# Kernel tuning notes

Hardware: AMD Instinct MI355X
Metric: run time of the kernel (lower is better)

The kernel has to match this reference:

```python
import jax, jax.numpy as jnp
import numpy as np

EPS = 1e-5  # torch BatchNorm default eps
B, C, T, NOUT, NCLS = 4096, 32, 512, 16, 4


def setup_inputs() -> dict:
    key = jax.random.key(0)
    ks = jax.random.split(key, 12)
    s = lambda k, shape: jax.random.normal(k, shape, jnp.float32) * 0.05
    return {
        "de": jax.random.normal(ks[0], (B, C, T), jnp.float32),
        "adj": jax.random.normal(ks[1], (B, C, C), jnp.float32),  # unused by forward (module recomputes corr)
        "dw_w": s(ks[2], (C, 1, 3)),      # depthwise Conv1d weight [C,1,3]
        "dw_b": s(ks[3], (C,)),
        "pw_w": s(ks[4], (C, C)),          # pointwise 1x1 conv [out,in]
        "pw_b": s(ks[5], (C,)),
        "bn1_g": jnp.ones((C,), jnp.float32),
        "bn1_b": jnp.zeros((C,), jnp.float32),
        "gc_w": s(ks[6], (T, NOUT)),       # GraphConvolution weight
        "fc_w": s(ks[7], (C * NOUT, C)),   # fc62 Linear(512,32)
        "fc_b": s(ks[8], (C,)),
        "bn2_g": jnp.ones((C,), jnp.float32),
        "bn2_b": jnp.zeros((C,), jnp.float32),
        "cls_w": s(ks[9], (C, NCLS)),      # fcclass Linear(32,4)
        "cls_b": s(ks[10], (NCLS,)),
    }


def reference(de, adj, dw_w, dw_b, pw_w, pw_b, bn1_g, bn1_b, gc_w,
              fc_w, fc_b, bn2_g, bn2_b, cls_w, cls_b):
    # --- SeparableConv2d (really 1d): depthwise k=3 -> pointwise 1x1 -> BN -> relu ---
    x = jax.lax.conv_general_dilated(
        de, dw_w, window_strides=(1,), padding=[(1, 1)],
        dimension_numbers=("NCH", "OIH", "NCH"),
        feature_group_count=de.shape[1]) + dw_b[None, :, None]
    x = jnp.einsum("oc,bct->bot", pw_w, x) + pw_b[None, :, None]
    m = x.mean((0, 2), keepdims=True)
    v = x.var((0, 2), keepdims=True)  # biased, as BN normalization uses
    x = (x - m) / jnp.sqrt(v + EPS) * bn1_g[None, :, None] + bn1_b[None, :, None]
    x = jax.nn.relu(x)                       # [B, C, T]

    # --- batched Pearson corrcoef over the time axis (vectorizes the per-sample loop) ---
    xt = x.transpose(0, 2, 1)                # [B, T, C]
    Tn = xt.shape[1]
    f = (Tn - 1) / Tn
    xc = xt - xt.mean(1, keepdims=True)
    num = jnp.einsum("btn,btm->bnm", xc, xc) / Tn   # biased covariance
    var = xt.var(1, ddof=1)                         # torch var default unbiased
    den = jnp.sqrt(var[:, :, None] * var[:, None, :]) * f
    cor = num / den                          # [B, C, C]

    # --- Chebyshev graph convolution (single K term, adj = cor) + relu ---
    g = jnp.einsum("bnm,bmt->bnt", cor, x)   # message passing over channel graph
    g = jax.nn.relu(jnp.einsum("bnt,to->bno", g, gc_w))  # [B, C, 16]

    # --- fc62: Linear -> BN1d -> (dropout: identity) -> sigmoid ---
    h = g.reshape(g.shape[0], -1) @ fc_w + fc_b          # [B, 32]
    m2 = h.mean(0)
    v2 = h.var(0)
    h = (h - m2) / jnp.sqrt(v2 + EPS) * bn2_g + bn2_b
    h = jax.nn.sigmoid(h)

    return h @ cls_w + cls_b                 # [B, 4]
```

## Files before the change

kernel.cpp:

```cpp
#include <hip/hip_runtime.h>
#include <math.h>

#define BB 4096
#define CC 32
#define TT 512
#define NOUTC 16
#define EPSF 1e-5f
#define XS 520


typedef __attribute__((ext_vector_type(16))) float f32x16;
typedef __attribute__((ext_vector_type(4)))  float f32x4;
typedef __attribute__((ext_vector_type(8)))  short short8;
typedef __attribute__((ext_vector_type(4)))  unsigned int u32x4;
typedef __attribute__((ext_vector_type(4)))  float vf4;
typedef vf4 __attribute__((aligned(4))) vf4u;

__device__ __forceinline__ unsigned short f2b(float f) {
  unsigned int u = __builtin_bit_cast(unsigned int, f);
  return (unsigned short)((u + 0x7FFFu + ((u >> 16) & 1u)) >> 16);
}
__device__ __forceinline__ float blo(unsigned int u) {
  return __builtin_bit_cast(float, u << 16);
}
__device__ __forceinline__ float bhi(unsigned int u) {
  return __builtin_bit_cast(float, u & 0xFFFF0000u);
}
__device__ __forceinline__ unsigned int pk2(float a, float b) {
  return (unsigned int)f2b(a) | ((unsigned int)f2b(b) << 16);
}

__device__ __forceinline__ void conv_cols(const float* __restrict__ deb,
    const float* __restrict__ dw, const float* __restrict__ db_,
    int tid, float* x1A, float* x1B) {
  int t0 = tid * 2;
  int off = (tid == 0) ? 0 : ((tid == 255) ? t0 - 2 : t0 - 1);
#pragma unroll
  for (int c = 0; c < CC; c++) {
    vf4u v = *reinterpret_cast<const vf4u*>(deb + c * TT + off);
    float vm1 = (tid == 0) ? 0.f : ((tid == 255) ? v.y : v.x);
    float v0  = (tid == 0) ? v.x : ((tid == 255) ? v.z : v.y);
    float vp1 = (tid == 0) ? v.y : ((tid == 255) ? v.w : v.z);
    float vp2 = (tid == 0) ? v.z : ((tid == 255) ? 0.f : v.w);
    float w0 = dw[c * 3], w1 = dw[c * 3 + 1], w2 = dw[c * 3 + 2], bc = db_[c];
    x1A[c] = fmaf(w0, vm1, fmaf(w1, v0, fmaf(w2, vp1, bc)));
    x1B[c] = fmaf(w0, v0, fmaf(w1, vp1, fmaf(w2, vp2, bc)));
  }
}

__device__ __forceinline__ void stage_row(unsigned short* lds1, int XHo, int XLo,
                                          int row, const float* x) {
#pragma unroll
  for (int cb = 0; cb < 4; cb++) {
    u32x4 hv, lv;
#pragma unroll
    for (int k = 0; k < 4; k++) {
      float a = x[cb * 8 + 2 * k], b2 = x[cb * 8 + 2 * k + 1];
      unsigned int ua = __builtin_bit_cast(unsigned int, a);
      unsigned int ub = __builtin_bit_cast(unsigned int, b2);
      hv[k] = (ua >> 16) | (ub & 0xFFFF0000u);
      float ra = a - __builtin_bit_cast(float, ua & 0xFFFF0000u);
      float rb = b2 - __builtin_bit_cast(float, ub & 0xFFFF0000u);
      lv[k] = pk2(ra, rb);
    }
    *(u32x4*)&lds1[XHo + row * 40 + cb * 8] = hv;
    *(u32x4*)&lds1[XLo + row * 40 + cb * 8] = lv;
  }
}

__global__ __launch_bounds__(256) void k1_stats(const float* __restrict__ de,
    const float* __restrict__ dw, const float* __restrict__ db_,
    const float* __restrict__ pw, const float* __restrict__ pwb,
    float* __restrict__ part, unsigned int* __restrict__ x2h, int useWs) {
  __shared__ __align__(16) unsigned short lds1[39168];
  const int XHo = 0, XLo = 10240, X2Bo = 20480, PWHo = 37120, PWLo = 38144;

  int tid = threadIdx.x, b = blockIdx.x;
  int lane = tid & 63, w = tid >> 6;
  int m31 = lane & 31, kh = lane >> 5;

  const float* deb = de + (size_t)b * CC * TT;
  float x1A[CC], x1B[CC];
  conv_cols(deb, dw, db_, tid, x1A, x1B);

  for (int i = tid; i < CC * CC; i += 256) {
    float v = pw[i];
    unsigned int u = __builtin_bit_cast(unsigned int, v);
    lds1[PWHo + i] = (unsigned short)(u >> 16);
    float r = v - __builtin_bit_cast(float, u & 0xFFFF0000u);
    lds1[PWLo + i] = f2b(r);
  }
  __syncthreads();

  short8 ah[2], al[2];
#pragma unroll
  for (int s = 0; s < 2; s++) {
    ah[s] = *(const short8*)&lds1[PWHo + m31 * 32 + s * 16 + kh * 8];
    al[s] = *(const short8*)&lds1[PWLo + m31 * 32 + s * 16 + kh * 8];
  }
  float pbv[16];
#pragma unroll
  for (int r = 0; r < 16; r++) pbv[r] = pwb[(r & 3) + 8 * (r >> 2) + 4 * kh];

#pragma unroll
  for (int h = 0; h < 2; h++) {
    if ((tid >> 7) == h) {
      int lr = 2 * (tid & 127);
      stage_row(lds1, XHo, XLo, lr, x1A);
      stage_row(lds1, XHo, XLo, lr + 1, x1B);
    }
    __syncthreads();

#pragma unroll
    for (int i = 0; i < 2; i++) {
      int wt = w * 2 + i;
      f32x16 acc;
#pragma unroll
      for (int r = 0; r < 16; r++) acc[r] = 0.f;
      int rowb = wt * 32 + m31;
#pragma unroll
      for (int s = 0; s < 2; s++) {
        short8 bh = *(const short8*)&lds1[XHo + rowb * 40 + s * 16 + kh * 8];
        short8 bl = *(const short8*)&lds1[XLo + rowb * 40 + s * 16 + kh * 8];
        acc = __builtin_amdgcn_mfma_f32_32x32x16_bf16(ah[s], bh, acc, 0, 0, 0);
        acc = __builtin_amdgcn_mfma_f32_32x32x16_bf16(ah[s], bl, acc, 0, 0, 0);
        acc = __builtin_amdgcn_mfma_f32_32x32x16_bf16(al[s], bh, acc, 0, 0, 0);
      }
      int t = h * 256 + wt * 32 + m31;
#pragma unroll
      for (int pr = 0; pr < 8; pr++) {
        int o0 = ((2 * pr) & 3) + 8 * (pr >> 1) + 4 * kh;
        unsigned int p = pk2(acc[2 * pr] + pbv[2 * pr], acc[2 * pr + 1] + pbv[2 * pr + 1]);
        lds1[X2Bo + o0 * 520 + t] = (unsigned short)(p & 0xFFFFu);
        lds1[X2Bo + (o0 + 1) * 520 + t] = (unsigned short)(p >> 16);
      }
    }
    __syncthreads();
  }

  unsigned int* xw = x2h + (size_t)b * (CC * 256);
  int L = tid & 63;
#pragma unroll
  for (int it = 0; it < 8; it++) {
    int o = it * 4 + w;
    u32x4 v = *(const u32x4*)&lds1[X2Bo + o * 520 + L * 8];
    float s = 0.f, q = 0.f;
#pragma unroll
    for (int k = 0; k < 4; k++) {
      float a = blo(v[k]), c2 = bhi(v[k]);
      s += a + c2;
      q = fmaf(a, a, fmaf(c2, c2, q));
    }
#pragma unroll
    for (int d = 1; d < 64; d <<= 1) { s += __shfl_xor(s, d); q += __shfl_xor(q, d); }
    if (L == 0) {
      part[(size_t)o * BB + b] = s;
      part[(size_t)(32 + o) * BB + b] = q;
    }
    if (useWs) *(u32x4*)(xw + (size_t)(it * 256 + tid) * 4) = v;
  }
}

__global__ void k2_bn1(const float* __restrict__ part, const float* __restrict__ g,
                       const float* __restrict__ bta, float* __restrict__ ws) {
  __shared__ float redS[256], redQ[256];
  int o = blockIdx.x, tid = threadIdx.x;
  const float* ps = part + (size_t)o * BB;
  const float* pq = part + (size_t)(CC + o) * BB;
  float s = 0, q = 0;
  for (int i = tid; i < BB; i += 256) { s += ps[i]; q += pq[i]; }
  redS[tid] = s; redQ[tid] = q;
  __syncthreads();
  for (int k = 128; k > 0; k >>= 1) {
    if (tid < k) { redS[tid] += redS[tid + k]; redQ[tid] += redQ[tid + k]; }
    __syncthreads();
  }
  if (tid == 0) {
    float N = (float)BB * (float)TT;
    float mean = redS[0] / N;
    float var = redQ[0] / N - mean * mean;
    float sc = g[o] / sqrtf(var + EPSF);
    ws[o] = sc;
    ws[32 + o] = bta[o] - mean * sc;
  }
}

__global__ __launch_bounds__(256) void k3_main(const float* __restrict__ de,
    const float* __restrict__ dw, const float* __restrict__ db_,
    const float* __restrict__ pw, const float* __restrict__ pwb,
    const float* __restrict__ ws, const float* __restrict__ gcw,
    const float* __restrict__ fcw, const float* __restrict__ fcb,
    float* __restrict__ hT, const unsigned int* __restrict__ x2h, int useWs) {
  __shared__ __align__(16) unsigned short x_s[CC * XS];
  __shared__ __align__(16) unsigned short gc_s[NOUTC * XS];
  __shared__ float gramP[2][CC * CC];
  __shared__ float zP[2][CC * NOUTC];
  __shared__ float num_s[CC * 33];
  __shared__ float red16[CC * 8];
  __shared__ float mu_s[CC], inv_s[CC];
  __shared__ float Zi_s[CC * NOUTC];
  __shared__ float g2_s[CC * NOUTC];
  __shared__ float red2[CC * 9];

  int tid = threadIdx.x, b = blockIdx.x;
  int w = tid >> 6, lane = tid & 63;
  int t0 = tid * 2;

  for (int i = tid; i < TT * NOUTC; i += 256) {
    int t = i >> 4, o = i & 15;
    gc_s[o * XS + t] = f2b(gcw[i]);
  }

  if (useWs) {
    const unsigned int* xr = x2h + (size_t)b * CC * 256;
#pragma unroll
    for (int o = 0; o < CC; o++) {
      unsigned int u = xr[o * 256 + tid];
      float sc = ws[o], sh = ws[32 + o];
      unsigned short hA = f2b(fmaxf(fmaf(blo(u), sc, sh), 0.f));
      unsigned short hB = f2b(fmaxf(fmaf(bhi(u), sc, sh), 0.f));
      *(unsigned int*)(&x_s[o * XS + t0]) = (unsigned int)hA | ((unsigned int)hB << 16);
    }
  } else {
    const float* deb = de + (size_t)b * CC * TT;
    float x1A[CC], x1B[CC];
    conv_cols(deb, dw, db_, tid, x1A, x1B);
#pragma unroll
    for (int o = 0; o < CC; o++) {
      float aA = pwb[o], aB = pwb[o];
#pragma unroll
      for (int c = 0; c < CC; c++) { float pv = pw[o * CC + c]; aA = fmaf(pv, x1A[c], aA); aB = fmaf(pv, x1B[c], aB); }
      float sc = ws[o], sh = ws[32 + o];
      unsigned short hA = f2b(fmaxf(fmaf(aA, sc, sh), 0.f));
      unsigned short hB = f2b(fmaxf(fmaf(aB, sc, sh), 0.f));
      *(unsigned int*)(&x_s[o * XS + t0]) = (unsigned int)hA | ((unsigned int)hB << 16);
    }
  }
  __syncthreads();

  {
    int c = tid >> 3, j = tid & 7;
    float s = 0.f;
#pragma unroll
    for (int it = 0; it < 8; it++) {
      u32x4 u = *reinterpret_cast<const u32x4*>(&x_s[c * XS + j * 64 + it * 8]);
#pragma unroll
      for (int k = 0; k < 4; k++) s += blo(u[k]) + bhi(u[k]);
    }
    red16[c * 8 + j] = s;
  }

  if (w < 2) {
    int m = lane & 31, kh = lane >> 5;
    f32x16 acc;
#pragma unroll
    for (int r = 0; r < 16; r++) acc[r] = 0.f;
    int kbase = w * 256 + kh * 8;
#pragma unroll
    for (int kk = 0; kk < 256; kk += 16) {
      short8 a = *(const short8*)(&x_s[m * XS + kbase + kk]);
      acc = __builtin_amdgcn_mfma_f32_32x32x16_bf16(a, a, acc, 0, 0, 0);
    }
#pragma unroll
    for (int r = 0; r < 16; r++) {
      int row = (r & 3) + 8 * (r >> 2) + 4 * kh;
      gramP[w][row * CC + m] = acc[r];
    }
  } else {
    int w2 = w - 2;
    int n16 = lane & 15, q = lane >> 4;
    f32x4 ac0, ac1;
#pragma unroll
    for (int r = 0; r < 4; r++) { ac0[r] = 0.f; ac1[r] = 0.f; }
    int kbase = w2 * 256 + q * 8;
#pragma unroll
    for (int kk = 0; kk < 256; kk += 32) {
      short8 bfr = *(const short8*)(&gc_s[n16 * XS + kbase + kk]);
      short8 af0 = *(const short8*)(&x_s[n16 * XS + kbase + kk]);
      short8 af1 = *(const short8*)(&x_s[(16 + n16) * XS + kbase + kk]);
      ac0 = __builtin_amdgcn_mfma_f32_16x16x32_bf16(af0, bfr, ac0, 0, 0, 0);
      ac1 = __builtin_amdgcn_mfma_f32_16x16x32_bf16(af1, bfr, ac1, 0, 0, 0);
    }
#pragma unroll
    for (int r = 0; r < 4; r++) {
      int row = q * 4 + r;
      zP[w2][row * NOUTC + n16] = ac0[r];
      zP[w2][(16 + row) * NOUTC + n16] = ac1[r];
    }
  }
  __syncthreads();
  if (tid < CC) {
    float s = 0.f;
#pragma unroll
    for (int j = 0; j < 8; j++) s += red16[tid * 8 + j];
    mu_s[tid] = s;
  }
  __syncthreads();
  for (int i = tid; i < CC * CC; i += 256) {
    int n = i >> 5, m = i & 31;
    num_s[n * 33 + m] = gramP[0][i] + gramP[1][i] - mu_s[n] * mu_s[m] * (1.f / (float)TT);
  }
  for (int i = tid; i < CC * NOUTC; i += 256) Zi_s[i] = zP[0][i] + zP[1][i];
  __syncthreads();
  if (tid < CC) inv_s[tid] = rsqrtf(num_s[tid * 33 + tid]);
  __syncthreads();
  for (int i = tid; i < CC * NOUTC; i += 256) {
    int n = i >> 4, o = i & 15;
    float s = 0.f;
#pragma unroll
    for (int m = 0; m < CC; m++) s = fmaf(num_s[n * 33 + m] * inv_s[m], Zi_s[m * NOUTC + o], s);
    g2_s[i] = fmaxf(s * inv_s[n], 0.f);
  }
  __syncthreads();
  {
    int j = tid & 31, ch = tid >> 5;
    float p = 0.f;
#pragma unroll
    for (int ii = 0; ii < 64; ii++) {
      int i = ch * 64 + ii;
      p = fmaf(g2_s[i], fcw[i * CC + j], p);
    }
    red2[j * 9 + ch] = p;
  }
  __syncthreads();
  if (tid < CC) {
    float h = fcb[tid];
#pragma unroll
    for (int ch = 0; ch < 8; ch++) h += red2[tid * 9 + ch];
    hT[(size_t)tid * BB + b] = h;
  }
}

__global__ void k4_bn2(const float* __restrict__ hT, const float* __restrict__ g,
                       const float* __restrict__ bta, float* __restrict__ ws) {
  __shared__ float redS[256], redQ[256];
  int j = blockIdx.x, tid = threadIdx.x;
  const float* row = hT + (size_t)j * BB;
  float s = 0, q = 0;
  for (int i = tid; i < BB; i += 256) { float v = row[i]; s += v; q = fmaf(v, v, q); }
  redS[tid] = s; redQ[tid] = q;
  __syncthreads();
  for (int k = 128; k > 0; k >>= 1) {
    if (tid < k) { redS[tid] += redS[tid + k]; redQ[tid] += redQ[tid + k]; }
    __syncthreads();
  }
  if (tid == 0) {
    float N = (float)BB;
    float mean = redS[0] / N;
    float var = redQ[0] / N - mean * mean;
    float sc = g[j] / sqrtf(var + EPSF);
    ws[64 + j] = sc;
    ws[96 + j] = bta[j] - mean * sc;
  }
}

__global__ void k5_out(const float* __restrict__ hT, const float* __restrict__ ws,
                       const float* __restrict__ clsw, const float* __restrict__ clsb,
                       float* __restrict__ out) {
  __shared__ float hs[CC * 257];
  int b0 = blockIdx.x * 256, tid = threadIdx.x;
  for (int i = tid; i < CC * 256; i += 256) {
    int j = i >> 8, bb = i & 255;
    float v = fmaf(hT[(size_t)j * BB + b0 + bb], ws[64 + j], ws[96 + j]);
    hs[j * 257 + bb] = 1.f / (1.f + expf(-v));
  }
  __syncthreads();
  float o0 = clsb[0], o1 = clsb[1], o2 = clsb[2], o3 = clsb[3];
#pragma unroll
  for (int j = 0; j < CC; j++) {
    float h = hs[j * 257 + tid];
    o0 = fmaf(h, clsw[j * 4 + 0], o0);
    o1 = fmaf(h, clsw[j * 4 + 1], o1);
    o2 = fmaf(h, clsw[j * 4 + 2], o2);
    o3 = fmaf(h, clsw[j * 4 + 3], o3);
  }
  float4* out4 = reinterpret_cast<float4*>(out);
  out4[b0 + tid] = make_float4(o0, o1, o2, o3);
}

extern "C" void kernel_launch(void* const* d_in, const int* in_sizes, int n_in,
                              void* d_out, int out_size, void* d_ws, size_t ws_size,
                              hipStream_t stream) {
  const float* de   = (const float*)d_in[0];
  const float* dw   = (const float*)d_in[2];
  const float* db_  = (const float*)d_in[3];
  const float* pw   = (const float*)d_in[4];
  const float* pwb  = (const float*)d_in[5];
  const float* bn1g = (const float*)d_in[6];
  const float* bn1b = (const float*)d_in[7];
  const float* gcw  = (const float*)d_in[8];
  const float* fcw  = (const float*)d_in[9];
  const float* fcb  = (const float*)d_in[10];
  const float* bn2g = (const float*)d_in[11];
  const float* bn2b = (const float*)d_in[12];
  const float* clsw = (const float*)d_in[13];
  const float* clsb = (const float*)d_in[14];

  float* ws   = (float*)d_ws;
  float* hT   = ws + 128;
  float* part = ws + 131200;
  unsigned int* x2h = (unsigned int*)(ws + 393344);
  float* out  = (float*)d_out;

  size_t need = 393344ull * 4ull + (size_t)BB * CC * 256 * 4;
  int useWs = (ws_size >= need) ? 1 : 0;

  k1_stats<<<BB, 256, 0, stream>>>(de, dw, db_, pw, pwb, part, x2h, useWs);
  k2_bn1<<<CC, 256, 0, stream>>>(part, bn1g, bn1b, ws);
  k3_main<<<BB, 256, 0, stream>>>(de, dw, db_, pw, pwb, ws, gcw, fcw, fcb, hT, x2h, useWs);
  k4_bn2<<<CC, 256, 0, stream>>>(hT, bn2g, bn2b, ws);
  k5_out<<<BB / 256, 256, 0, stream>>>(hT, ws, clsw, clsb, out);
}
```

Measured before the change: 521.4 us.

## Use single fp16 MFMA for pointwise conv, shrink LDS, pre-swizzle GCN weights

The pointwise conv in k1 switches from a three-pass bf16 hi/lo split to a single fp16 MFMA pass. This cuts the MFMA count and roughly halves LDS use. The stats reduction now runs per half and writes the workspace in a half-major layout. The GCN weight is converted to bf16 once in k2, in MFMA fragment order, so k3 reads it straight into registers instead of rebuilding gc_s every block. Both big kernels trim LDS and set launch_bounds(256,3) to raise occupancy. The cost is reduced precision for the pointwise result: fp16 range and mantissa replace the near-fp32 split.

Result: faster. 487.0 us (-6.6%).

```diff
diff --git a/kernel.cpp b/kernel.cpp
--- a/kernel.cpp
+++ b/kernel.cpp
@@ -12,6 +12,7 @@
 typedef __attribute__((ext_vector_type(16))) float f32x16;
 typedef __attribute__((ext_vector_type(4)))  float f32x4;
 typedef __attribute__((ext_vector_type(8)))  short short8;
+typedef __attribute__((ext_vector_type(8)))  _Float16 half8;
 typedef __attribute__((ext_vector_type(4)))  unsigned int u32x4;
 typedef __attribute__((ext_vector_type(4)))  float vf4;
 typedef vf4 __attribute__((aligned(4))) vf4u;
@@ -28,6 +29,13 @@
 }
 __device__ __forceinline__ unsigned int pk2(float a, float b) {
   return (unsigned int)f2b(a) | ((unsigned int)f2b(b) << 16);
+}
+__device__ __forceinline__ unsigned short h16(float f) {
+  _Float16 h = (_Float16)f;
+  return __builtin_bit_cast(unsigned short, h);
+}
+__device__ __forceinline__ unsigned int h2pk(float a, float b) {
+  return (unsigned int)h16(a) | ((unsigned int)h16(b) << 16);
 }
 
 __device__ __forceinline__ void conv_cols(const float* __restrict__ deb,
@@ -48,66 +56,52 @@
   }
 }
 
-__device__ __forceinline__ void stage_row(unsigned short* lds1, int XHo, int XLo,
-                                          int row, const float* x) {
+__device__ __forceinline__ void stage_row_f16(unsigned short* lds1, int row, const float* x) {
 #pragma unroll
   for (int cb = 0; cb < 4; cb++) {
-    u32x4 hv, lv;
-#pragma unroll
-    for (int k = 0; k < 4; k++) {
-      float a = x[cb * 8 + 2 * k], b2 = x[cb * 8 + 2 * k + 1];
-      unsigned int ua = __builtin_bit_cast(unsigned int, a);
-      unsigned int ub = __builtin_bit_cast(unsigned int, b2);
-      hv[k] = (ua >> 16) | (ub & 0xFFFF0000u);
-      float ra = a - __builtin_bit_cast(float, ua & 0xFFFF0000u);
-      float rb = b2 - __builtin_bit_cast(float, ub & 0xFFFF0000u);
-      lv[k] = pk2(ra, rb);
-    }
-    *(u32x4*)&lds1[XHo + row * 40 + cb * 8] = hv;
-    *(u32x4*)&lds1[XLo + row * 40 + cb * 8] = lv;
-  }
-}
-
-__global__ __launch_bounds__(256) void k1_stats(const float* __restrict__ de,
+    u32x4 v;
+#pragma unroll
+    for (int k = 0; k < 4; k++) v[k] = h2pk(x[cb * 8 + 2 * k], x[cb * 8 + 2 * k + 1]);
+    *(u32x4*)&lds1[row * 40 + cb * 8] = v;
+  }
+}
+
+__global__ __launch_bounds__(256, 3) void k1_stats(const float* __restrict__ de,
     const float* __restrict__ dw, const float* __restrict__ db_,
     const float* __restrict__ pw, const float* __restrict__ pwb,
     float* __restrict__ part, unsigned int* __restrict__ x2h, int useWs) {
-  __shared__ __align__(16) unsigned short lds1[39168];
-  const int XHo = 0, XLo = 10240, X2Bo = 20480, PWHo = 37120, PWLo = 38144;
+  __shared__ __align__(16) unsigned short lds1[19712];
+  const int XFo = 0, X2Bo = 10240, PWFo = 18688;
 
   int tid = threadIdx.x, b = blockIdx.x;
   int lane = tid & 63, w = tid >> 6;
   int m31 = lane & 31, kh = lane >> 5;
+  int hw = tid >> 5, l32 = tid & 31;
 
   const float* deb = de + (size_t)b * CC * TT;
   float x1A[CC], x1B[CC];
   conv_cols(deb, dw, db_, tid, x1A, x1B);
 
-  for (int i = tid; i < CC * CC; i += 256) {
-    float v = pw[i];
-    unsigned int u = __builtin_bit_cast(unsigned int, v);
-    lds1[PWHo + i] = (unsigned short)(u >> 16);
-    float r = v - __builtin_bit_cast(float, u & 0xFFFF0000u);
-    lds1[PWLo + i] = f2b(r);
-  }
-  __syncthreads();
-
-  short8 ah[2], al[2];
-#pragma unroll
-  for (int s = 0; s < 2; s++) {
-    ah[s] = *(const short8*)&lds1[PWHo + m31 * 32 + s * 16 + kh * 8];
-    al[s] = *(const short8*)&lds1[PWLo + m31 * 32 + s * 16 + kh * 8];
-  }
+  for (int i = tid; i < CC * CC; i += 256) lds1[PWFo + i] = h16(pw[i]);
+  __syncthreads();
+
+  half8 ah[2];
+#pragma unroll
+  for (int s = 0; s < 2; s++)
+    ah[s] = *(const half8*)&lds1[PWFo + m31 * 32 + s * 16 + kh * 8];
   float pbv[16];
 #pragma unroll
   for (int r = 0; r < 16; r++) pbv[r] = pwb[(r & 3) + 8 * (r >> 2) + 4 * kh];
+
+  unsigned int* xw = x2h + (size_t)b * (CC * 256);
+  float sAcc[4] = {0.f, 0.f, 0.f, 0.f}, qAcc[4] = {0.f, 0.f, 0.f, 0.f};
 
 #pragma unroll
   for (int h = 0; h < 2; h++) {
     if ((tid >> 7) == h) {
       int lr = 2 * (tid & 127);
-      stage_row(lds1, XHo, XLo, lr, x1A);
-      stage_row(lds1, XHo, XLo, lr + 1, x1B);
+      stage_row_f16(lds1, lr, x1A);
+      stage_row_f16(lds1, lr + 1, x1B);
     }
     __syncthreads();
 
@@ -120,51 +114,60 @@
       int rowb = wt * 32 + m31;
 #pragma unroll
       for (int s = 0; s < 2; s++) {
-        short8 bh = *(const short8*)&lds1[XHo + rowb * 40 + s * 16 + kh * 8];
-        short8 bl = *(const short8*)&lds1[XLo + rowb * 40 + s * 16 + kh * 8];
-        acc = __builtin_amdgcn_mfma_f32_32x32x16_bf16(ah[s], bh, acc, 0, 0, 0);
-        acc = __builtin_amdgcn_mfma_f32_32x32x16_bf16(ah[s], bl, acc, 0, 0, 0);
-        acc = __builtin_amdgcn_mfma_f32_32x32x16_bf16(al[s], bh, acc, 0, 0, 0);
+        half8 bh = *(const half8*)&lds1[XFo + rowb * 40 + s * 16 + kh * 8];
+        acc = __builtin_amdgcn_mfma_f32_32x32x16_f16(ah[s], bh, acc, 0, 0, 0);
       }
-      int t = h * 256 + wt * 32 + m31;
+      int tloc = wt * 32 + m31;
 #pragma unroll
       for (int pr = 0; pr < 8; pr++) {
         int o0 = ((2 * pr) & 3) + 8 * (pr >> 1) + 4 * kh;
         unsigned int p = pk2(acc[2 * pr] + pbv[2 * pr], acc[2 * pr + 1] + pbv[2 * pr + 1]);
-        lds1[X2Bo + o0 * 520 + t] = (unsigned short)(p & 0xFFFFu);
-        lds1[X2Bo + (o0 + 1) * 520 + t] = (unsigned short)(p >> 16);
+        lds1[X2Bo + o0 * 264 + tloc] = (unsigned short)(p & 0xFFFFu);
+        lds1[X2Bo + (o0 + 1) * 264 + tloc] = (unsigned short)(p >> 16);
       }
     }
     __syncthreads();
-  }
-
-  unsigned int* xw = x2h + (size_t)b * (CC * 256);
-  int L = tid & 63;
-#pragma unroll
-  for (int it = 0; it < 8; it++) {
-    int o = it * 4 + w;
-    u32x4 v = *(const u32x4*)&lds1[X2Bo + o * 520 + L * 8];
-    float s = 0.f, q = 0.f;
-#pragma unroll
-    for (int k = 0; k < 4; k++) {
-      float a = blo(v[k]), c2 = bhi(v[k]);
-      s += a + c2;
-      q = fmaf(a, a, fmaf(c2, c2, q));
-    }
-#pragma unroll
-    for (int d = 1; d < 64; d <<= 1) { s += __shfl_xor(s, d); q += __shfl_xor(q, d); }
-    if (L == 0) {
-      part[(size_t)o * BB + b] = s;
-      part[(size_t)(32 + o) * BB + b] = q;
-    }
-    if (useWs) *(u32x4*)(xw + (size_t)(it * 256 + tid) * 4) = v;
+
+#pragma unroll
+    for (int it = 0; it < 4; it++) {
+      int o = it * 8 + hw;
+      u32x4 v = *(const u32x4*)&lds1[X2Bo + o * 264 + l32 * 8];
+      float s = 0.f, q = 0.f;
+#pragma unroll
+      for (int k = 0; k < 4; k++) {
+        float a = blo(v[k]), c2 = bhi(v[k]);
+        s += a + c2;
+        q = fmaf(a, a, fmaf(c2, c2, q));
+      }
+#pragma unroll
+      for (int d = 1; d < 32; d <<= 1) { s += __shfl_xor(s, d); q += __shfl_xor(q, d); }
+      sAcc[it] += s; qAcc[it] += q;
+      if (useWs) *(u32x4*)(xw + (size_t)h * 4096 + o * 128 + l32 * 4) = v;
+    }
+  }
+
+  if (l32 == 0) {
+#pragma unroll
+    for (int it = 0; it < 4; it++) {
+      int o = it * 8 + hw;
+      part[(size_t)o * BB + b] = sAcc[it];
+      part[(size_t)(32 + o) * BB + b] = qAcc[it];
+    }
   }
 }
 
 __global__ void k2_bn1(const float* __restrict__ part, const float* __restrict__ g,
-                       const float* __restrict__ bta, float* __restrict__ ws) {
+                       const float* __restrict__ bta, float* __restrict__ ws,
+                       const float* __restrict__ gcw, unsigned short* __restrict__ gcf) {
   __shared__ float redS[256], redQ[256];
   int o = blockIdx.x, tid = threadIdx.x;
+  {
+    int i = o * 256 + tid;
+    int e = i & 7, ln = (i >> 3) & 63, j = (i >> 9) & 7, w2 = i >> 12;
+    int q = ln >> 4, n16 = ln & 15;
+    int t = w2 * 256 + q * 8 + j * 32 + e;
+    gcf[i] = f2b(gcw[t * 16 + n16]);
+  }
   const float* ps = part + (size_t)o * BB;
   const float* pq = part + (size_t)(CC + o) * BB;
   float s = 0, q = 0;
@@ -185,37 +188,28 @@
   }
 }
 
-__global__ __launch_bounds__(256) void k3_main(const float* __restrict__ de,
+__global__ __launch_bounds__(256, 3) void k3_main(const float* __restrict__ de,
     const float* __restrict__ dw, const float* __restrict__ db_,
     const float* __restrict__ pw, const float* __restrict__ pwb,
-    const float* __restrict__ ws, const float* __restrict__ gcw,
+    const float* __restrict__ ws, const unsigned short* __restrict__ gcf,
     const float* __restrict__ fcw, const float* __restrict__ fcb,
     float* __restrict__ hT, const unsigned int* __restrict__ x2h, int useWs) {
   __shared__ __align__(16) unsigned short x_s[CC * XS];
-  __shared__ __align__(16) unsigned short gc_s[NOUTC * XS];
   __shared__ float gramP[2][CC * CC];
   __shared__ float zP[2][CC * NOUTC];
-  __shared__ float num_s[CC * 33];
   __shared__ float red16[CC * 8];
   __shared__ float mu_s[CC], inv_s[CC];
-  __shared__ float Zi_s[CC * NOUTC];
-  __shared__ float g2_s[CC * NOUTC];
-  __shared__ float red2[CC * 9];
 
   int tid = threadIdx.x, b = blockIdx.x;
   int w = tid >> 6, lane = tid & 63;
   int t0 = tid * 2;
 
-  for (int i = tid; i < TT * NOUTC; i += 256) {
-    int t = i >> 4, o = i & 15;
-    gc_s[o * XS + t] = f2b(gcw[i]);
-  }
-
   if (useWs) {
-    const unsigned int* xr = x2h + (size_t)b * CC * 256;
+    const unsigned int* xr = x2h + (size_t)b * (CC * 256);
+    int base = (tid >> 7) * 4096 + (tid & 127);
 #pragma unroll
     for (int o = 0; o < CC; o++) {
-      unsigned int u = xr[o * 256 + tid];
+      unsigned int u = xr[base + o * 128];
       float sc = ws[o], sh = ws[32 + o];
       unsigned short hA = f2b(fmaxf(fmaf(blo(u), sc, sh), 0.f));
       unsigned short hB = f2b(fmaxf(fmaf(bhi(u), sc, sh), 0.f));
@@ -272,14 +266,18 @@
     f32x4 ac0, ac1;
 #pragma unroll
     for (int r = 0; r < 4; r++) { ac0[r] = 0.f; ac1[r] = 0.f; }
+    const unsigned short* gf = gcf + w2 * 4096;
+    short8 bfr[8];
+#pragma unroll
+    for (int j = 0; j < 8; j++) bfr[j] = *(const short8*)(gf + (j * 64 + lane) * 8);
     int kbase = w2 * 256 + q * 8;
 #pragma unroll
-    for (int kk = 0; kk < 256; kk += 32) {
-      short8 bfr = *(const short8*)(&gc_s[n16 * XS + kbase + kk]);
+    for (int j = 0; j < 8; j++) {
+      int kk = j * 32;
       short8 af0 = *(const short8*)(&x_s[n16 * XS + kbase + kk]);
       short8 af1 = *(const short8*)(&x_s[(16 + n16) * XS + kbase + kk]);
-      ac0 = __builtin_amdgcn_mfma_f32_16x16x32_bf16(af0, bfr, ac0, 0, 0, 0);
-      ac1 = __builtin_amdgcn_mfma_f32_16x16x32_bf16(af1, bfr, ac1, 0, 0, 0);
+      ac0 = __builtin_amdgcn_mfma_f32_16x16x32_bf16(af0, bfr[j], ac0, 0, 0, 0);
+      ac1 = __builtin_amdgcn_mfma_f32_16x16x32_bf16(af1, bfr[j], ac1, 0, 0, 0);
     }
 #pragma unroll
     for (int r = 0; r < 4; r++) {
@@ -296,29 +294,33 @@
     mu_s[tid] = s;
   }
   __syncthreads();
+  float* gram0 = gramP[0];
+  float* Zi = zP[0];
+  float* g2 = zP[1];
   for (int i = tid; i < CC * CC; i += 256) {
     int n = i >> 5, m = i & 31;
-    num_s[n * 33 + m] = gramP[0][i] + gramP[1][i] - mu_s[n] * mu_s[m] * (1.f / (float)TT);
-  }
-  for (int i = tid; i < CC * NOUTC; i += 256) Zi_s[i] = zP[0][i] + zP[1][i];
-  __syncthreads();
-  if (tid < CC) inv_s[tid] = rsqrtf(num_s[tid * 33 + tid]);
+    gram0[i] = gram0[i] + gramP[1][i] - mu_s[n] * mu_s[m] * (1.f / (float)TT);
+  }
+  for (int i = tid; i < CC * NOUTC; i += 256) Zi[i] = zP[0][i] + zP[1][i];
+  __syncthreads();
+  if (tid < CC) inv_s[tid] = rsqrtf(gram0[tid * 32 + tid]);
   __syncthreads();
   for (int i = tid; i < CC * NOUTC; i += 256) {
     int n = i >> 4, o = i & 15;
     float s = 0.f;
 #pragma unroll
-    for (int m = 0; m < CC; m++) s = fmaf(num_s[n * 33 + m] * inv_s[m], Zi_s[m * NOUTC + o], s);
-    g2_s[i] = fmaxf(s * inv_s[n], 0.f);
-  }
-  __syncthreads();
+    for (int m = 0; m < CC; m++) s = fmaf(gram0[n * 32 + m] * inv_s[m], Zi[m * NOUTC + o], s);
+    g2[i] = fmaxf(s * inv_s[n], 0.f);
+  }
+  __syncthreads();
+  float* red2 = gramP[1];
   {
     int j = tid & 31, ch = tid >> 5;
     float p = 0.f;
 #pragma unroll
     for (int ii = 0; ii < 64; ii++) {
       int i = ch * 64 + ii;
-      p = fmaf(g2_s[i], fcw[i * CC + j], p);
+      p = fmaf(g2[i], fcw[i * CC + j], p);
     }
     red2[j * 9 + ch] = p;
   }
@@ -396,18 +398,19 @@
   const float* clsw = (const float*)d_in[13];
   const float* clsb = (const float*)d_in[14];
 
-  float* ws   = (float*)d_ws;
-  float* hT   = ws + 128;
-  float* part = ws + 131200;
-  unsigned int* x2h = (unsigned int*)(ws + 393344);
+  float* ws = (float*)d_ws;
+  unsigned short* gcf = (unsigned short*)(ws + 128);
+  float* hT   = ws + 4224;
+  float* part = ws + 135296;
+  unsigned int* x2h = (unsigned int*)(ws + 397440);
   float* out  = (float*)d_out;
 
-  size_t need = 393344ull * 4ull + (size_t)BB * CC * 256 * 4;
+  size_t need = ((size_t)397440 + 33554432ull) * 4ull;
   int useWs = (ws_size >= need) ? 1 : 0;
 
   k1_stats<<<BB, 256, 0, stream>>>(de, dw, db_, pw, pwb, part, x2h, useWs);
-  k2_bn1<<<CC, 256, 0, stream>>>(part, bn1g, bn1b, ws);
-  k3_main<<<BB, 256, 0, stream>>>(de, dw, db_, pw, pwb, ws, gcw, fcw, fcb, hT, x2h, useWs);
+  k2_bn1<<<CC, 256, 0, stream>>>(part, bn1g, bn1b, ws, gcw, gcf);
+  k3_main<<<BB, 256, 0, stream>>>(de, dw, db_, pw, pwb, ws, gcf, fcw, fcb, hT, x2h, useWs);
   k4_bn2<<<CC, 256, 0, stream>>>(hT, bn2g, bn2b, ws);
   k5_out<<<BB / 256, 256, 0, stream>>>(hT, ws, clsw, clsb, out);
 }
```
